# Optimization experiments

Hardware: AMD Instinct MI355X
Metric: run time of the kernel (lower is better)

Reference implementation:

```python
import jax, jax.numpy as jnp
import numpy as np

EMBED_DIM = 768
NUM_HEADS = 12
HEAD_DIM = EMBED_DIM // NUM_HEADS
BSZ = 8
N_NODE = 512


def setup_inputs() -> dict:
    key = jax.random.key(0)
    ks = jax.random.split(key, 12)
    s = 0.02
    E = EMBED_DIM
    return {
        "query": jax.random.normal(ks[0], (N_NODE, BSZ, E), jnp.float32),
        "attention_bias": jax.random.normal(ks[1], (BSZ, NUM_HEADS, N_NODE, N_NODE), jnp.float32),
        "node_position": jax.random.normal(ks[2], (BSZ, N_NODE, 3), jnp.float32),
        "Wq": jax.random.normal(ks[3], (E, E), jnp.float32) * s,
        "bq": jnp.zeros((E,), jnp.float32),
        "Wk": jax.random.normal(ks[4], (E, E), jnp.float32) * s,
        "bk": jnp.zeros((E,), jnp.float32),
        "Wv": jax.random.normal(ks[5], (E, E), jnp.float32) * s,
        "bv": jnp.zeros((E,), jnp.float32),
        "W1": jax.random.normal(ks[6], (E, 1), jnp.float32) * s,
        "b1": jnp.zeros((1,), jnp.float32),
        "W2": jax.random.normal(ks[7], (E, 1), jnp.float32) * s,
        "b2": jnp.zeros((1,), jnp.float32),
        "W3": jax.random.normal(ks[8], (E, 1), jnp.float32) * s,
        "b3": jnp.zeros((1,), jnp.float32),
    }


def reference(query, attention_bias, node_position, Wq, bq, Wk, bk, Wv, bv,
              W1, b1, W2, b2, W3, b3):
    bsz, n = node_position.shape[:2]
    H = attention_bias.shape[1]
    E = query.shape[-1]
    hd = E // H
    scaling = hd ** -0.5

    # unit direction vectors between node pairs: delta[b,i,j] = pos[j]-pos[i]
    delta = node_position[:, None, :, :] - node_position[:, :, None, :]  # (b,n,n,3)
    dist = jnp.linalg.norm(delta, axis=-1)                               # (b,n,n)
    delta = delta / (dist[..., None] + 1e-5)

    x = jnp.swapaxes(query, 0, 1)  # (b,n,E)
    q = (x @ Wq + bq).reshape(bsz, n, H, hd).transpose(0, 2, 1, 3) * scaling  # (b,h,n,d)
    k = (x @ Wk + bk).reshape(bsz, n, H, hd).transpose(0, 2, 1, 3)
    v = (x @ Wv + bv).reshape(bsz, n, H, hd).transpose(0, 2, 1, 3)

    attn = jnp.einsum('bhid,bhjd->bhij', q, k)
    probs = jax.nn.softmax(attn + attention_bias, axis=-1)  # (b,h,i,j); dropout = identity (eval)

    # rotational aggregation: out[b,i,c,h,d] = sum_j probs[b,h,i,j]*delta[b,i,j,c]*v[b,h,j,d]
    xo = jnp.einsum('bhij,bijc,bhjd->bichd', probs, delta, v).reshape(bsz, n, 3, E)

    f1 = xo[:, :, 0, :] @ W1 + b1  # (b,n,1)
    f2 = xo[:, :, 1, :] @ W2 + b2
    f3 = xo[:, :, 2, :] @ W3 + b3
    return jnp.concatenate([f1, f2, f3], axis=-1).astype(jnp.float32)  # (b,n,3)
```

## Files before the change

### kernel.cpp

```cpp
#include <hip/hip_runtime.h>
#include <math.h>

#define EDIM 768
#define NH 12
#define HD 64
#define BSZ 8
#define NN 512
#define NCAT 1664

typedef short short8 __attribute__((ext_vector_type(8)));
typedef float f32x4 __attribute__((ext_vector_type(4)));

__device__ __forceinline__ unsigned short f2bf(float x) {
    unsigned int u = __float_as_uint(x);
    u = (u + 0x7FFF + ((u >> 16) & 1)) >> 16;
    return (unsigned short)u;
}
__device__ __forceinline__ float bf2f(unsigned short s) {
    return __uint_as_float(((unsigned int)s) << 16);
}
__device__ __forceinline__ void gl2lds16(const void* g, void* l) {
    __builtin_amdgcn_global_load_lds(
        (const __attribute__((address_space(1))) unsigned int*)g,
        (__attribute__((address_space(3))) unsigned int*)l, 16, 0, 0);
}

#define PB_GEOM_END 512
#define PB_TR_END   1664
#define PB_VW_END   1772
#define PB_CVT_END  3308
#define PB_BC_END   3315
#define PREP_BLOCKS 3350

__global__ __launch_bounds__(256) void k_prep(
        const float* __restrict__ query, const float* __restrict__ pos,
        const float* __restrict__ Wq, const float* __restrict__ bq,
        const float* __restrict__ Wk, const float* __restrict__ bk,
        const float* __restrict__ Wv, const float* __restrict__ bv,
        const float* __restrict__ W1, const float* __restrict__ W2,
        const float* __restrict__ W3,
        unsigned short* __restrict__ WT, float* __restrict__ bcat,
        unsigned short* __restrict__ Xb,
        unsigned short* __restrict__ ud0, unsigned short* __restrict__ ud1,
        unsigned short* __restrict__ ud2) {
    __shared__ float sm[1536];
    const int bid = blockIdx.x;
    const int t = threadIdx.x;

    if (bid < PB_GEOM_END) {
        float* psx = sm; float* psy = sm + NN; float* psz = sm + 2 * NN;
        const int b = bid >> 6, i0 = (bid & 63) * 8;
        for (int idx = t; idx < NN; idx += 256) {
            const float* p = pos + ((size_t)b * NN + idx) * 3;
            psx[idx] = p[0]; psy[idx] = p[1]; psz[idx] = p[2];
        }
        __syncthreads();
        const int i = i0 + (t >> 5);
        const float qx = psx[i], qy = psy[i], qz = psz[i];
        const size_t row = ((size_t)b * NN + i) * NN;
        for (int jt = 0; jt < 4; jt++) {
            int j = ((t & 31) + jt * 32) * 4;
            unsigned short s0[4], s1[4], s2[4];
            #pragma unroll
            for (int u = 0; u < 4; u++) {
                float dx = psx[j + u] - qx, dy = psy[j + u] - qy, dz = psz[j + u] - qz;
                float inv = 1.f / (sqrtf(dx * dx + dy * dy + dz * dz) + 1e-5f);
                s0[u] = f2bf(dx * inv); s1[u] = f2bf(dy * inv); s2[u] = f2bf(dz * inv);
            }
            *(uint2*)&ud0[row + j] = make_uint2(s0[0] | ((unsigned)s0[1] << 16), s0[2] | ((unsigned)s0[3] << 16));
            *(uint2*)&ud1[row + j] = make_uint2(s1[0] | ((unsigned)s1[1] << 16), s1[2] | ((unsigned)s1[3] << 16));
            *(uint2*)&ud2[row + j] = make_uint2(s2[0] | ((unsigned)s2[1] << 16), s2[2] | ((unsigned)s2[3] << 16));
        }
    } else if (bid < PB_TR_END) {
        float (*tile)[33] = (float(*)[33])sm;
        const int tb = bid - PB_GEOM_END;
        const int n0 = (tb % 48) * 32, e0 = (tb / 48) * 32;
        const float* src = (n0 < 768) ? Wq : Wk;
        const int ol0 = (n0 < 768) ? n0 : (n0 - 768);
        const int tx = t & 31, ty = t >> 5;
        #pragma unroll
        for (int s = 0; s < 4; s++)
            tile[ty + s * 8][tx] = src[(size_t)(e0 + ty + s * 8) * EDIM + ol0 + tx];
        __syncthreads();
        #pragma unroll
        for (int s = 0; s < 4; s++)
            WT[(size_t)(n0 + ty + s * 8) * EDIM + e0 + tx] = f2bf(tile[tx][ty + s * 8]);
    } else if (bid < PB_VW_END) {
        int idx = (bid - PB_TR_END) * 256 + t;
        int o2 = idx / 768, e = idx - o2 * 768;
        int h = o2 / 3, c = o2 - (o2 / 3) * 3;
        const float* Wc = (c == 0) ? W1 : (c == 1) ? W2 : W3;
        float s = 0.f;
        #pragma unroll 8
        for (int d = 0; d < HD; d++) s += Wv[(size_t)e * EDIM + h * HD + d] * Wc[h * HD + d];
        WT[(size_t)(1536 + o2) * EDIM + e] = f2bf(s);
    } else if (bid < PB_CVT_END) {
        int idx = (bid - PB_VW_END) * 256 + t;
        int m = idx / 96, e8 = (idx - (idx / 96) * 96) * 8;
        int b = m >> 9, i = m & (NN - 1);
        const float* src = query + ((size_t)i * BSZ + b) * EDIM + e8;
        float4 v0 = *(const float4*)src;
        float4 v1 = *(const float4*)(src + 4);
        unsigned int p0 = f2bf(v0.x) | ((unsigned int)f2bf(v0.y) << 16);
        unsigned int p1 = f2bf(v0.z) | ((unsigned int)f2bf(v0.w) << 16);
        unsigned int p2 = f2bf(v1.x) | ((unsigned int)f2bf(v1.y) << 16);
        unsigned int p3 = f2bf(v1.z) | ((unsigned int)f2bf(v1.w) << 16);
        uint4 pk = {p0, p1, p2, p3};
        *(uint4*)&Xb[(size_t)idx * 8] = pk;
    } else if (bid < PB_BC_END) {
        int o = (bid - PB_CVT_END) * 256 + t;
        if (o < NCAT) {
            float v = 0.f;
            if (o < 768) v = bq[o];
            else if (o < 1536) v = bk[o - 768];
            else if (o < 1572) {
                int o2 = o - 1536;
                int h = o2 / 3, c = o2 - (o2 / 3) * 3;
                const float* Wc = (c == 0) ? W1 : (c == 1) ? W2 : W3;
                float s = 0.f;
                for (int d = 0; d < HD; d++) s += bv[h * HD + d] * Wc[h * HD + d];
                v = s;
            }
            bcat[o] = v;
        }
    } else {
        int tid = (bid - PB_BC_END) * 256 + t;
        if (tid < 8832) {
            uint4 z = {0, 0, 0, 0};
            *(uint4*)&WT[(size_t)1572 * EDIM + (size_t)tid * 8] = z;
        }
    }
}

__global__ __launch_bounds__(256) void k_gemm_qkv(
        const unsigned short* __restrict__ Xb, const unsigned short* __restrict__ WT,
        const float* __restrict__ bcat,
        unsigned short* __restrict__ qb, unsigned short* __restrict__ kb,
        float* __restrict__ vwb) {
    __shared__ short As[8 * 64 * 8];
    __shared__ short Bs[8 * 128 * 8];
    const int t = threadIdx.x;
    const int m0 = blockIdx.x * 64, n0 = blockIdx.y * 128;
    const int w = t >> 6, lane = t & 63, quad = lane >> 4, ln = lane & 15;
    const int wm = (w & 1) * 32, wn = (w >> 1) * 64;

    f32x4 acc[2][4];
    #pragma unroll
    for (int mi = 0; mi < 2; mi++)
        #pragma unroll
        for (int ni = 0; ni < 4; ni++) acc[mi][ni] = (f32x4){0.f, 0.f, 0.f, 0.f};

    for (int k0 = 0; k0 < EDIM; k0 += 64) {
        __syncthreads();
        #pragma unroll
        for (int is = 0; is < 2; is++) {
            int slot = is * 256 + t;
            int g = slot >> 6, m = slot & 63;
            gl2lds16(Xb + (size_t)(m0 + m) * EDIM + k0 + g * 8, &As[(size_t)(is * 256 + w * 64) * 8]);
        }
        #pragma unroll
        for (int is = 0; is < 4; is++) {
            int slot = is * 256 + t;
            int g = slot >> 7, n = slot & 127;
            gl2lds16(WT + (size_t)(n0 + n) * EDIM + k0 + g * 8, &Bs[(size_t)(is * 256 + w * 64) * 8]);
        }
        __syncthreads();
        #pragma unroll
        for (int s = 0; s < 2; s++) {
            short8 af[2], bf[4];
            #pragma unroll
            for (int mi = 0; mi < 2; mi++)
                af[mi] = *(const short8*)&As[(size_t)((s * 4 + quad) * 64 + wm + mi * 16 + ln) * 8];
            #pragma unroll
            for (int ni = 0; ni < 4; ni++)
                bf[ni] = *(const short8*)&Bs[(size_t)((s * 4 + quad) * 128 + wn + ni * 16 + ln) * 8];
            #pragma unroll
            for (int mi = 0; mi < 2; mi++)
                #pragma unroll
                for (int ni = 0; ni < 4; ni++)
                    acc[mi][ni] = __builtin_amdgcn_mfma_f32_16x16x32_bf16(af[mi], bf[ni], acc[mi][ni], 0, 0, 0);
        }
    }

    #pragma unroll
    for (int mi = 0; mi < 2; mi++) {
        #pragma unroll
        for (int r = 0; r < 4; r++) {
            int mg = m0 + wm + mi * 16 + quad * 4 + r;
            int b_ = mg >> 9, i_ = mg & (NN - 1);
            #pragma unroll
            for (int ni = 0; ni < 4; ni++) {
                int o = n0 + wn + ni * 16 + ln;
                float val = acc[mi][ni][r] + bcat[o];
                if (o < 768) {
                    int h = o >> 6, d = o & 63;
                    qb[(((size_t)b_ * NH + h) * NN + i_) * HD + d] = f2bf(val * 0.125f);
                } else if (o < 1536) {
                    int o2 = o - 768;
                    int h = o2 >> 6, d = o2 & 63;
                    kb[(((size_t)b_ * NH + h) * NN + i_) * HD + d] = f2bf(val);
                } else if (o < 1572) {
                    int o2 = o - 1536;
                    int h = o2 / 3, c = o2 - (o2 / 3) * 3;
                    vwb[(((size_t)b_ * NH + h) * NN + i_) * 3 + c] = val;
                }
            }
        }
    }
}

__global__ __launch_bounds__(256) void k_attn(
        const unsigned short* __restrict__ qb, const unsigned short* __restrict__ kb,
        const float* __restrict__ vwb, const float* __restrict__ bias,
        const unsigned short* __restrict__ ud0, const unsigned short* __restrict__ ud1,
        const unsigned short* __restrict__ ud2,
        float* __restrict__ mp, float* __restrict__ lp,
        float* __restrict__ a0p, float* __restrict__ a1p, float* __restrict__ a2p) {
    __shared__ short Ks[8 * 64 * 8];
    __shared__ float ws0[NN], ws1[NN], ws2[NN];

    const int t = threadIdx.x;
    const int bid = blockIdx.x;
    const int h = bid % NH;
    const int r1 = bid / NH;
    const int js = r1 & 3;
    const int it = (r1 >> 2) & 7;
    const int b = r1 >> 5;
    const int i0 = it * 64;
    const int jb = js * 128;
    const int w = t >> 6, lane = t & 63, quad = lane >> 4, ln = lane & 15;
    const size_t bh = (size_t)b * NH + h;

    for (int idx = t; idx < NN * 3; idx += 256) {
        float v = vwb[bh * (NN * 3) + idx];
        int j = idx / 3, c = idx - (idx / 3) * 3;
        if (c == 0) ws0[j] = v; else if (c == 1) ws1[j] = v; else ws2[j] = v;
    }

    const int ig = i0 + w * 16 + ln;
    const unsigned short* qrow = qb + (bh * NN + ig) * HD;
    short8 qf0 = *(const short8*)(qrow + quad * 8);
    short8 qf1 = *(const short8*)(qrow + 32 + quad * 8);
    const float* brow = bias + (bh * NN + ig) * NN;
    const size_t udrow = ((size_t)b * NN + ig) * NN;

    float m_r = -3.0e38f, l_r = 0.f, a0 = 0.f, a1 = 0.f, a2 = 0.f;

    for (int jt = 0; jt < 2; jt++) {
        const int j0 = jb + jt * 64;
        __syncthreads();
        #pragma unroll
        for (int is = 0; is < 2; is++) {
            int slot = is * 256 + t;
            int dg = slot >> 6, j = slot & 63;
            gl2lds16(kb + (bh * NN + j0 + j) * HD + dg * 8, &Ks[(size_t)(is * 256 + w * 64) * 8]);
        }
        __syncthreads();

        f32x4 acc[4];
        #pragma unroll
        for (int sub = 0; sub < 4; sub++) {
            short8 af0 = *(const short8*)&Ks[(size_t)(quad * 64 + sub * 16 + ln) * 8];
            short8 af1 = *(const short8*)&Ks[(size_t)((4 + quad) * 64 + sub * 16 + ln) * 8];
            f32x4 z = {0.f, 0.f, 0.f, 0.f};
            z = __builtin_amdgcn_mfma_f32_16x16x32_bf16(af0, qf0, z, 0, 0, 0);
            z = __builtin_amdgcn_mfma_f32_16x16x32_bf16(af1, qf1, z, 0, 0, 0);
            acc[sub] = z;
        }

        float sv[16];
        #pragma unroll
        for (int sub = 0; sub < 4; sub++) {
            f32x4 bv = *(const f32x4*)(brow + j0 + sub * 16 + quad * 4);
            sv[sub * 4 + 0] = acc[sub][0] + bv[0];
            sv[sub * 4 + 1] = acc[sub][1] + bv[1];
            sv[sub * 4 + 2] = acc[sub][2] + bv[2];
            sv[sub * 4 + 3] = acc[sub][3] + bv[3];
        }
        float lm = sv[0];
        #pragma unroll
        for (int u = 1; u < 16; u++) lm = fmaxf(lm, sv[u]);
        float mn = fmaxf(m_r, lm);
        float alpha = __expf(m_r - mn);
        float lps = 0.f, s0 = 0.f, s1 = 0.f, s2 = 0.f;
        #pragma unroll
        for (int sub = 0; sub < 4; sub++) {
            int j = j0 + sub * 16 + quad * 4;
            f32x4 w0v = *(const f32x4*)&ws0[j];
            f32x4 w1v = *(const f32x4*)&ws1[j];
            f32x4 w2v = *(const f32x4*)&ws2[j];
            union { uint2 u; unsigned short s[4]; } U0, U1, U2;
            U0.u = *(const uint2*)&ud0[udrow + j];
            U1.u = *(const uint2*)&ud1[udrow + j];
            U2.u = *(const uint2*)&ud2[udrow + j];
            #pragma unroll
            for (int r = 0; r < 4; r++) {
                float p = __expf(sv[sub * 4 + r] - mn);
                lps += p;
                s0 = fmaf(p * bf2f(U0.s[r]), w0v[r], s0);
                s1 = fmaf(p * bf2f(U1.s[r]), w1v[r], s1);
                s2 = fmaf(p * bf2f(U2.s[r]), w2v[r], s2);
            }
        }
        l_r = l_r * alpha + lps;
        a0 = a0 * alpha + s0;
        a1 = a1 * alpha + s1;
        a2 = a2 * alpha + s2;
        m_r = mn;
    }

    #pragma unroll
    for (int off = 16; off <= 32; off <<= 1) {
        float mo = __shfl_xor(m_r, off, 64);
        float lo = __shfl_xor(l_r, off, 64);
        float b0 = __shfl_xor(a0, off, 64);
        float b1 = __shfl_xor(a1, off, 64);
        float b2 = __shfl_xor(a2, off, 64);
        float mn = fmaxf(m_r, mo);
        float e1 = __expf(m_r - mn), e2 = __expf(mo - mn);
        l_r = l_r * e1 + lo * e2;
        a0 = a0 * e1 + b0 * e2;
        a1 = a1 * e1 + b1 * e2;
        a2 = a2 * e1 + b2 * e2;
        m_r = mn;
    }
    if (quad == 0) {
        size_t o4 = (bh * NN + ig) * 4 + js;
        mp[o4] = m_r; lp[o4] = l_r;
        a0p[o4] = a0; a1p[o4] = a1; a2p[o4] = a2;
    }
}

__global__ __launch_bounds__(256) void k_finalize(
        const float* __restrict__ mp, const float* __restrict__ lp,
        const float* __restrict__ a0p, const float* __restrict__ a1p,
        const float* __restrict__ a2p,
        const float* __restrict__ b1, const float* __restrict__ b2,
        const float* __restrict__ b3, float* __restrict__ out) {
    int idx = blockIdx.x * 256 + threadIdx.x;
    int b = idx >> 9, i = idx & (NN - 1);
    float s0 = 0.f, s1 = 0.f, s2 = 0.f;
    #pragma unroll
    for (int h = 0; h < NH; h++) {
        size_t base = (((size_t)b * NH + h) * NN + i) * 4;
        f32x4 mv = *(const f32x4*)&mp[base];
        f32x4 lv = *(const f32x4*)&lp[base];
        f32x4 A0 = *(const f32x4*)&a0p[base];
        f32x4 A1 = *(const f32x4*)&a1p[base];
        f32x4 A2 = *(const f32x4*)&a2p[base];
        float M = fmaxf(fmaxf(mv[0], mv[1]), fmaxf(mv[2], mv[3]));
        float L = 0.f, c0 = 0.f, c1 = 0.f, c2 = 0.f;
        #pragma unroll
        for (int js = 0; js < 4; js++) {
            float e = __expf(mv[js] - M);
            L = fmaf(e, lv[js], L);
            c0 = fmaf(e, A0[js], c0);
            c1 = fmaf(e, A1[js], c1);
            c2 = fmaf(e, A2[js], c2);
        }
        float inv = 1.f / L;
        s0 = fmaf(c0, inv, s0);
        s1 = fmaf(c1, inv, s1);
        s2 = fmaf(c2, inv, s2);
    }
    float* op = out + (size_t)idx * 3;
    op[0] = s0 + b1[0];
    op[1] = s1 + b2[0];
    op[2] = s2 + b3[0];
}

extern "C" void kernel_launch(void* const* d_in, const int* in_sizes, int n_in,
                              void* d_out, int out_size, void* d_ws, size_t ws_size,
                              hipStream_t stream) {
    const float* query = (const float*)d_in[0];
    const float* bias  = (const float*)d_in[1];
    const float* pos   = (const float*)d_in[2];
    const float* Wq = (const float*)d_in[3];
    const float* bq = (const float*)d_in[4];
    const float* Wk = (const float*)d_in[5];
    const float* bk = (const float*)d_in[6];
    const float* Wv = (const float*)d_in[7];
    const float* bv = (const float*)d_in[8];
    const float* W1 = (const float*)d_in[9];
    const float* b1 = (const float*)d_in[10];
    const float* W2 = (const float*)d_in[11];
    const float* b2 = (const float*)d_in[12];
    const float* W3 = (const float*)d_in[13];
    const float* b3 = (const float*)d_in[14];
    float* out = (float*)d_out;

    char* p = (char*)d_ws;
    unsigned short* WT = (unsigned short*)p; p += (size_t)NCAT * EDIM * 2;
    float* bcat = (float*)p;                 p += (size_t)NCAT * 4;
    unsigned short* Xb = (unsigned short*)p; p += (size_t)BSZ * NN * EDIM * 2;
    unsigned short* qb = (unsigned short*)p; p += (size_t)BSZ * NH * NN * HD * 2;
    unsigned short* kb = (unsigned short*)p; p += (size_t)BSZ * NH * NN * HD * 2;
    float* vwb = (float*)p;                  p += (size_t)BSZ * NH * NN * 3 * 4;
    unsigned short* ud0 = (unsigned short*)p; p += (size_t)BSZ * NN * NN * 2;
    unsigned short* ud1 = (unsigned short*)p; p += (size_t)BSZ * NN * NN * 2;
    unsigned short* ud2 = (unsigned short*)p; p += (size_t)BSZ * NN * NN * 2;
    const size_t PSZ = (size_t)BSZ * NH * NN * 4;
    float* mp  = (float*)p; p += PSZ * 4;
    float* lp  = (float*)p; p += PSZ * 4;
    float* a0p = (float*)p; p += PSZ * 4;
    float* a1p = (float*)p; p += PSZ * 4;
    float* a2p = (float*)p; p += PSZ * 4;

    k_prep<<<PREP_BLOCKS, 256, 0, stream>>>(query, pos, Wq, bq, Wk, bk, Wv, bv,
                                            W1, W2, W3, WT, bcat, Xb, ud0, ud1, ud2);
    dim3 g2(64, 13);
    k_gemm_qkv<<<g2, 256, 0, stream>>>(Xb, WT, bcat, qb, kb, vwb);
    k_attn<<<BSZ * NH * 8 * 4, 256, 0, stream>>>(qb, kb, vwb, bias, ud0, ud1, ud2,
                                                 mp, lp, a0p, a1p, a2p);
    k_finalize<<<BSZ * NN / 256, 256, 0, stream>>>(mp, lp, a0p, a1p, a2p, b1, b2, b3, out);
}
```

Measured before the change: 288.3 us.

## Load full 128-key K slab at once and use single-pass softmax in attention

The attention kernel now stages both 64-key K tiles into LDS in one go, before the vwb staging and Q loads. It preloads the bias into the MFMA accumulators and computes an exact row max across the quads before one exp/accumulate pass. The old two-iteration online softmax and its rescaling merges are replaced by plain shuffle sums, and LDS for ws arrays is shrunk to only the needed 128-key slice. It also adds a min-blocks occupancy hint and vectorises the Wv·Wc fold in the prep kernel. The cost is more registers for 8 accumulators and a larger K buffer.

```diff
diff --git a/kernel.cpp b/kernel.cpp
--- a/kernel.cpp
+++ b/kernel.cpp
@@ -90,9 +90,14 @@
         int o2 = idx / 768, e = idx - o2 * 768;
         int h = o2 / 3, c = o2 - (o2 / 3) * 3;
         const float* Wc = (c == 0) ? W1 : (c == 1) ? W2 : W3;
+        const float4* wvp = (const float4*)(Wv + (size_t)e * EDIM + h * HD);
+        const float4* wcp = (const float4*)(Wc + h * HD);
         float s = 0.f;
-        #pragma unroll 8
-        for (int d = 0; d < HD; d++) s += Wv[(size_t)e * EDIM + h * HD + d] * Wc[h * HD + d];
+        #pragma unroll
+        for (int d4 = 0; d4 < 16; d4++) {
+            float4 a = wvp[d4], b = wcp[d4];
+            s += a.x * b.x + a.y * b.y + a.z * b.z + a.w * b.w;
+        }
         WT[(size_t)(1536 + o2) * EDIM + e] = f2bf(s);
     } else if (bid < PB_CVT_END) {
         int idx = (bid - PB_VW_END) * 256 + t;
@@ -209,15 +214,15 @@
     }
 }
 
-__global__ __launch_bounds__(256) void k_attn(
+__global__ __launch_bounds__(256, 4) void k_attn(
         const unsigned short* __restrict__ qb, const unsigned short* __restrict__ kb,
         const float* __restrict__ vwb, const float* __restrict__ bias,
         const unsigned short* __restrict__ ud0, const unsigned short* __restrict__ ud1,
         const unsigned short* __restrict__ ud2,
         float* __restrict__ mp, float* __restrict__ lp,
         float* __restrict__ a0p, float* __restrict__ a1p, float* __restrict__ a2p) {
-    __shared__ short Ks[8 * 64 * 8];
-    __shared__ float ws0[NN], ws1[NN], ws2[NN];
+    __shared__ short Ks[2 * 8 * 64 * 8];
+    __shared__ float ws0[128], ws1[128], ws2[128];
 
     const int t = threadIdx.x;
     const int bid = blockIdx.x;
@@ -231,98 +236,79 @@
     const int w = t >> 6, lane = t & 63, quad = lane >> 4, ln = lane & 15;
     const size_t bh = (size_t)b * NH + h;
 
-    for (int idx = t; idx < NN * 3; idx += 256) {
-        float v = vwb[bh * (NN * 3) + idx];
-        int j = idx / 3, c = idx - (idx / 3) * 3;
-        if (c == 0) ws0[j] = v; else if (c == 1) ws1[j] = v; else ws2[j] = v;
+    #pragma unroll
+    for (int is = 0; is < 4; is++) {
+        int slot = is * 256 + t;
+        int tile = slot >> 9, dg = (slot >> 6) & 7, j = slot & 63;
+        gl2lds16(kb + (bh * NN + jb + tile * 64 + j) * HD + dg * 8,
+                 &Ks[(size_t)(is * 256 + w * 64) * 8]);
+    }
+    for (int idx = t; idx < 384; idx += 256) {
+        float v = vwb[bh * (NN * 3) + (size_t)jb * 3 + idx];
+        int jj = idx / 3, c = idx - (idx / 3) * 3;
+        if (c == 0) ws0[jj] = v; else if (c == 1) ws1[jj] = v; else ws2[jj] = v;
     }
 
     const int ig = i0 + w * 16 + ln;
     const unsigned short* qrow = qb + (bh * NN + ig) * HD;
     short8 qf0 = *(const short8*)(qrow + quad * 8);
     short8 qf1 = *(const short8*)(qrow + 32 + quad * 8);
-    const float* brow = bias + (bh * NN + ig) * NN;
-    const size_t udrow = ((size_t)b * NN + ig) * NN;
-
-    float m_r = -3.0e38f, l_r = 0.f, a0 = 0.f, a1 = 0.f, a2 = 0.f;
-
-    for (int jt = 0; jt < 2; jt++) {
-        const int j0 = jb + jt * 64;
-        __syncthreads();
-        #pragma unroll
-        for (int is = 0; is < 2; is++) {
-            int slot = is * 256 + t;
-            int dg = slot >> 6, j = slot & 63;
-            gl2lds16(kb + (bh * NN + j0 + j) * HD + dg * 8, &Ks[(size_t)(is * 256 + w * 64) * 8]);
-        }
-        __syncthreads();
-
-        f32x4 acc[4];
-        #pragma unroll
-        for (int sub = 0; sub < 4; sub++) {
-            short8 af0 = *(const short8*)&Ks[(size_t)(quad * 64 + sub * 16 + ln) * 8];
-            short8 af1 = *(const short8*)&Ks[(size_t)((4 + quad) * 64 + sub * 16 + ln) * 8];
-            f32x4 z = {0.f, 0.f, 0.f, 0.f};
-            z = __builtin_amdgcn_mfma_f32_16x16x32_bf16(af0, qf0, z, 0, 0, 0);
-            z = __builtin_amdgcn_mfma_f32_16x16x32_bf16(af1, qf1, z, 0, 0, 0);
-            acc[sub] = z;
-        }
-
-        float sv[16];
-        #pragma unroll
-        for (int sub = 0; sub < 4; sub++) {
-            f32x4 bv = *(const f32x4*)(brow + j0 + sub * 16 + quad * 4);
-            sv[sub * 4 + 0] = acc[sub][0] + bv[0];
-            sv[sub * 4 + 1] = acc[sub][1] + bv[1];
-            sv[sub * 4 + 2] = acc[sub][2] + bv[2];
-            sv[sub * 4 + 3] = acc[sub][3] + bv[3];
-        }
-        float lm = sv[0];
-        #pragma unroll
-        for (int u = 1; u < 16; u++) lm = fmaxf(lm, sv[u]);
-        float mn = fmaxf(m_r, lm);
-        float alpha = __expf(m_r - mn);
-        float lps = 0.f, s0 = 0.f, s1 = 0.f, s2 = 0.f;
-        #pragma unroll
-        for (int sub = 0; sub < 4; sub++) {
-            int j = j0 + sub * 16 + quad * 4;
-            f32x4 w0v = *(const f32x4*)&ws0[j];
-            f32x4 w1v = *(const f32x4*)&ws1[j];
-            f32x4 w2v = *(const f32x4*)&ws2[j];
-            union { uint2 u; unsigned short s[4]; } U0, U1, U2;
-            U0.u = *(const uint2*)&ud0[udrow + j];
-            U1.u = *(const uint2*)&ud1[udrow + j];
-            U2.u = *(const uint2*)&ud2[udrow + j];
-            #pragma unroll
-            for (int r = 0; r < 4; r++) {
-                float p = __expf(sv[sub * 4 + r] - mn);
-                lps += p;
-                s0 = fmaf(p * bf2f(U0.s[r]), w0v[r], s0);
-                s1 = fmaf(p * bf2f(U1.s[r]), w1v[r], s1);
-                s2 = fmaf(p * bf2f(U2.s[r]), w2v[r], s2);
-            }
-        }
-        l_r = l_r * alpha + lps;
-        a0 = a0 * alpha + s0;
-        a1 = a1 * alpha + s1;
-        a2 = a2 * alpha + s2;
-        m_r = mn;
+    const float* brow = bias + (bh * NN + ig) * NN + jb;
+    const size_t udrow = ((size_t)b * NN + ig) * NN + jb;
+
+    f32x4 acc[8];
+    #pragma unroll
+    for (int s8 = 0; s8 < 8; s8++) {
+        int off = (s8 >> 2) * 64 + (s8 & 3) * 16 + quad * 4;
+        acc[s8] = *(const f32x4*)(brow + off);
+    }
+
+    __syncthreads();
+
+    #pragma unroll
+    for (int s8 = 0; s8 < 8; s8++) {
+        int tile = s8 >> 2, sub = s8 & 3;
+        short8 af0 = *(const short8*)&Ks[(size_t)((tile * 8 + quad) * 64 + sub * 16 + ln) * 8];
+        short8 af1 = *(const short8*)&Ks[(size_t)((tile * 8 + 4 + quad) * 64 + sub * 16 + ln) * 8];
+        acc[s8] = __builtin_amdgcn_mfma_f32_16x16x32_bf16(af0, qf0, acc[s8], 0, 0, 0);
+        acc[s8] = __builtin_amdgcn_mfma_f32_16x16x32_bf16(af1, qf1, acc[s8], 0, 0, 0);
+    }
+
+    float m_r = acc[0][0];
+    #pragma unroll
+    for (int s8 = 0; s8 < 8; s8++)
+        #pragma unroll
+        for (int r = 0; r < 4; r++) m_r = fmaxf(m_r, acc[s8][r]);
+    m_r = fmaxf(m_r, __shfl_xor(m_r, 16, 64));
+    m_r = fmaxf(m_r, __shfl_xor(m_r, 32, 64));
+
+    float l_r = 0.f, a0 = 0.f, a1 = 0.f, a2 = 0.f;
+    #pragma unroll
+    for (int s8 = 0; s8 < 8; s8++) {
+        int off = (s8 >> 2) * 64 + (s8 & 3) * 16 + quad * 4;
+        f32x4 w0v = *(const f32x4*)&ws0[off];
+        f32x4 w1v = *(const f32x4*)&ws1[off];
+        f32x4 w2v = *(const f32x4*)&ws2[off];
+        union { uint2 u; unsigned short s[4]; } U0, U1, U2;
+        U0.u = *(const uint2*)&ud0[udrow + off];
+        U1.u = *(const uint2*)&ud1[udrow + off];
+        U2.u = *(const uint2*)&ud2[udrow + off];
+        #pragma unroll
+        for (int r = 0; r < 4; r++) {
+            float p = __expf(acc[s8][r] - m_r);
+            l_r += p;
+            a0 = fmaf(p * bf2f(U0.s[r]), w0v[r], a0);
+            a1 = fmaf(p * bf2f(U1.s[r]), w1v[r], a1);
+            a2 = fmaf(p * bf2f(U2.s[r]), w2v[r], a2);
+        }
     }
 
     #pragma unroll
     for (int off = 16; off <= 32; off <<= 1) {
-        float mo = __shfl_xor(m_r, off, 64);
-        float lo = __shfl_xor(l_r, off, 64);
-        float b0 = __shfl_xor(a0, off, 64);
-        float b1 = __shfl_xor(a1, off, 64);
-        float b2 = __shfl_xor(a2, off, 64);
-        float mn = fmaxf(m_r, mo);
-        float e1 = __expf(m_r - mn), e2 = __expf(mo - mn);
-        l_r = l_r * e1 + lo * e2;
-        a0 = a0 * e1 + b0 * e2;
-        a1 = a1 * e1 + b1 * e2;
-        a2 = a2 * e1 + b2 * e2;
-        m_r = mn;
+        l_r += __shfl_xor(l_r, off, 64);
+        a0  += __shfl_xor(a0, off, 64);
+        a1  += __shfl_xor(a1, off, 64);
+        a2  += __shfl_xor(a2, off, 64);
     }
     if (quad == 0) {
         size_t o4 = (bh * NN + ig) * 4 + js;
```

Result: faster. 281.3 us (-2.4%).
